# Performance work log

Hardware: AMD Instinct MI355X
Metric: run time of the kernel (lower is better)

The kernel has to match this reference:

```python
import jax, jax.numpy as jnp
import numpy as np

EMBED_DIM = 1024
NUM_HEADS = 16
HEAD_DIM = EMBED_DIM // NUM_HEADS
SCALING = HEAD_DIM ** -0.5
ATTN_CONST = 3.032639477052158
BSZ, SEQ = 4, 1024


def setup_inputs() -> dict:
    key = jax.random.key(0)
    ks = jax.random.split(key, 12)
    s = EMBED_DIM ** -0.5
    return {
        "hidden_states": jax.random.normal(ks[0], (BSZ, SEQ, EMBED_DIM), jnp.float32),
        "attn_input_ids": jax.random.uniform(ks[1], (BSZ * NUM_HEADS, SEQ, SEQ), jnp.float32),
        "Wq": jax.random.normal(ks[2], (EMBED_DIM, EMBED_DIM), jnp.float32) * s,
        "bq": jax.random.normal(ks[3], (EMBED_DIM,), jnp.float32) * 0.02,
        "Wk": jax.random.normal(ks[4], (EMBED_DIM, EMBED_DIM), jnp.float32) * s,
        "bk": jax.random.normal(ks[5], (EMBED_DIM,), jnp.float32) * 0.02,
        "Wv": jax.random.normal(ks[6], (EMBED_DIM, EMBED_DIM), jnp.float32) * s,
        "bv": jax.random.normal(ks[7], (EMBED_DIM,), jnp.float32) * 0.02,
        "Wo": jax.random.normal(ks[8], (EMBED_DIM, EMBED_DIM), jnp.float32) * s,
        "bo": jax.random.normal(ks[9], (EMBED_DIM,), jnp.float32) * 0.02,
    }


def _heads(x, bsz, seq):
    # (b, s, e) -> (b, h, s, d)
    return x.reshape(bsz, seq, NUM_HEADS, HEAD_DIM).transpose(0, 2, 1, 3)


def reference(hidden_states, attn_input_ids, Wq, bq, Wk, bk, Wv, bv, Wo, bo):
    bsz, tgt_len, embed_dim = hidden_states.shape
    # torch nn.Linear: y = x @ W.T + b
    q = (hidden_states @ Wq.T + bq) * SCALING
    k = hidden_states @ Wk.T + bk
    v = hidden_states @ Wv.T + bv
    q = _heads(q, bsz, tgt_len)   # (b,h,t,d)
    k = _heads(k, bsz, tgt_len)
    v = _heads(v, bsz, tgt_len)
    # scores: (b,h,t,s)
    scores = jnp.einsum('bhtd,bhsd->bhts', q, k)
    # additive bias: ATTN_FUNCTION(attn_input_ids) = ATTN_CONST * attn_input_ids
    bias = (ATTN_CONST * attn_input_ids).reshape(bsz, NUM_HEADS, tgt_len, tgt_len)
    attn = jax.nn.softmax(scores + bias, axis=-1)
    # dropout p=0.0 / eval mode -> identity
    out = jnp.einsum('bhts,bhsd->bhtd', attn, v)
    out = out.transpose(0, 2, 1, 3).reshape(bsz, tgt_len, embed_dim)
    return out @ Wo.T + bo
```

## Files before the change

kernel.cpp:

```cpp
#include <hip/hip_runtime.h>
#include <stdint.h>

#define BSZ 4
#define SEQ 1024
#define EMB 1024
#define NH 16
#define HD 64

static constexpr float kScaling   = 0.125f;
static constexpr float kAttnConst = 3.032639477052158f;

using u16 = unsigned short;
typedef __attribute__((ext_vector_type(8))) short  frag8;
typedef __attribute__((ext_vector_type(4))) float  floatx4;
typedef __attribute__((ext_vector_type(4))) u16    u16x4;

__device__ inline float bf2f(u16 v) {
  uint32_t u = ((uint32_t)v) << 16;
  return __builtin_bit_cast(float, u);
}
__device__ inline u16 f2bf(float x) {
  uint32_t u = __builtin_bit_cast(uint32_t, x);
  u += 0x7fffu + ((u >> 16) & 1u);
  return (u16)(u >> 16);
}

__global__ __launch_bounds__(256)
void cvt_kernel(const float* __restrict__ H,
                const float* __restrict__ Wq, const float* __restrict__ Wk,
                const float* __restrict__ Wv, const float* __restrict__ Wo,
                u16* __restrict__ Xb,
                u16* __restrict__ Wqb, u16* __restrict__ Wkb,
                u16* __restrict__ Wvb, u16* __restrict__ Wob)
{
  const size_t base = ((size_t)blockIdx.x * 256 + threadIdx.x) * 4;
  const size_t HN = (size_t)BSZ * SEQ * EMB;
  const size_t WN = (size_t)EMB * EMB;
  const float* src;
  u16* dst;
  size_t off;
  if (base < HN) {
    src = H; dst = Xb; off = base;
  } else {
    const size_t r = base - HN;
    const int w = (int)(r >> 20);
    off = r & (WN - 1);
    src = (w == 0) ? Wq : (w == 1) ? Wk : (w == 2) ? Wv : Wo;
    dst = (w == 0) ? Wqb : (w == 1) ? Wkb : (w == 2) ? Wvb : Wob;
  }
  const float4 v = *reinterpret_cast<const float4*>(src + off);
  u16x4 o;
  o[0] = f2bf(v.x); o[1] = f2bf(v.y); o[2] = f2bf(v.z); o[3] = f2bf(v.w);
  *reinterpret_cast<u16x4*>(dst + off) = o;
}

__device__ inline void gemm_mainloop(const u16* __restrict__ X,
                                     const u16* __restrict__ W,
                                     int m0, int n0,
                                     u16* As, u16* Bs,
                                     floatx4 acc[4][4])
{
  const int tid  = threadIdx.x;
  const int wave = tid >> 6;
  const int lane = tid & 63;
  const int l15  = lane & 15;
  const int quad = lane >> 4;
  const int wr   = (wave >> 1) * 64;
  const int wc   = (wave & 1) * 64;
  const int srow = wave * 32 + (lane >> 3);
  const int scol = (lane & 7) * 8;

  for (int i = 0; i < 4; ++i)
    for (int j = 0; j < 4; ++j)
      acc[i][j] = (floatx4){0.f, 0.f, 0.f, 0.f};

  for (int k0 = 0; k0 < EMB; k0 += 64) {
    for (int i = 0; i < 4; ++i) {
      const u16* ga = X + (size_t)(m0 + srow + i * 8) * EMB + k0 + scol;
      const u16* gb = W + (size_t)(n0 + srow + i * 8) * EMB + k0 + scol;
      u16* la = As + (wave * 4 + i) * 512;
      u16* lb = Bs + (wave * 4 + i) * 512;
      __builtin_amdgcn_global_load_lds(
          (__attribute__((address_space(1))) void*)ga,
          (__attribute__((address_space(3))) void*)la, 16, 0, 0);
      __builtin_amdgcn_global_load_lds(
          (__attribute__((address_space(1))) void*)gb,
          (__attribute__((address_space(3))) void*)lb, 16, 0, 0);
    }
    __syncthreads();
    for (int kc = 0; kc < 2; ++kc) {
      frag8 af[4], bfr[4];
      for (int i = 0; i < 4; ++i)
        af[i] = *reinterpret_cast<const frag8*>(
            As + (wr + i * 16 + l15) * 64 + kc * 32 + quad * 8);
      for (int j = 0; j < 4; ++j)
        bfr[j] = *reinterpret_cast<const frag8*>(
            Bs + (wc + j * 16 + l15) * 64 + kc * 32 + quad * 8);
      for (int i = 0; i < 4; ++i)
        for (int j = 0; j < 4; ++j)
          acc[i][j] = __builtin_amdgcn_mfma_f32_16x16x32_bf16(
              af[i], bfr[j], acc[i][j], 0, 0, 0);
    }
    __syncthreads();
  }
}

__global__ __launch_bounds__(256, 3)
void qkv_kernel(const u16* __restrict__ X,
                const u16* __restrict__ Wqb, const float* __restrict__ bq,
                const u16* __restrict__ Wkb, const float* __restrict__ bk,
                const u16* __restrict__ Wvb, const float* __restrict__ bv,
                u16* __restrict__ Qs, u16* __restrict__ Ks, u16* __restrict__ Vt)
{
  __shared__ __align__(16) u16 As[128 * 64];
  __shared__ __align__(16) u16 Bs[128 * 64];
  const int z  = blockIdx.z;
  const u16*   W  = (z == 0) ? Wqb : (z == 1) ? Wkb : Wvb;
  const float* bb = (z == 0) ? bq  : (z == 1) ? bk  : bv;
  const int m0 = blockIdx.y * 128;
  const int n0 = blockIdx.x * 128;

  floatx4 acc[4][4];
  gemm_mainloop(X, W, m0, n0, As, Bs, acc);

  const int lane = threadIdx.x & 63, l15 = lane & 15, quad = lane >> 4;
  const int wave = threadIdx.x >> 6;
  const int wr = (wave >> 1) * 64, wc = (wave & 1) * 64;

  for (int j = 0; j < 4; ++j) {
    const int   n  = n0 + wc + j * 16 + l15;
    const float bn = bb[n];
    for (int i = 0; i < 4; ++i) {
      const int mbase = m0 + wr + i * 16 + quad * 4;
      if (z == 2) {
        const int b = mbase >> 10, t = mbase & 1023;
        const int h = n >> 6,      d = n & 63;
        u16x4 pk;
        for (int r = 0; r < 4; ++r) pk[r] = f2bf(acc[i][j][r] + bn);
        *reinterpret_cast<u16x4*>(
            Vt + ((size_t)((b * NH + h) * HD + d)) * SEQ + t) = pk;
      } else {
        u16* dst = (z == 0) ? Qs : Ks;
        const float sc = (z == 0) ? kScaling : 1.0f;
        for (int r = 0; r < 4; ++r)
          dst[(size_t)(mbase + r) * EMB + n] = f2bf((acc[i][j][r] + bn) * sc);
      }
    }
  }
}

__global__ __launch_bounds__(256, 4)
void attn_kernel(const u16* __restrict__ Qs, const u16* __restrict__ Ks,
                 const u16* __restrict__ Vt, const float* __restrict__ bias,
                 u16* __restrict__ ctx)
{
  __shared__ __align__(16) u16 Kt[64 * 64];
  __shared__ __align__(16) u16 Vs[64 * 64];
  __shared__ __align__(16) u16 Pbuf[64 * 72];
  const int bh = blockIdx.x;
  const int b  = bh >> 4;
  const int h  = bh & 15;
  const int t0 = blockIdx.y * 64;
  const int wave = threadIdx.x >> 6;
  const int lane = threadIdx.x & 63;
  const int l15 = lane & 15, quad = lane >> 4;
  const int wrow = t0 + wave * 16;
  const int srow = wave * 16 + (lane >> 3);
  const int scol = (lane & 7) * 8;

  frag8 qf[2];
  for (int kc = 0; kc < 2; ++kc)
    qf[kc] = *reinterpret_cast<const frag8*>(
        Qs + (size_t)(b * SEQ + wrow + l15) * EMB + h * HD + kc * 32 + quad * 8);

  floatx4 O[4];
  for (int df = 0; df < 4; ++df) O[df] = (floatx4){0.f, 0.f, 0.f, 0.f};
  float rs[4] = {0.f, 0.f, 0.f, 0.f};

  const float* bline = bias + ((size_t)bh * SEQ + wrow + quad * 4) * SEQ + l15;

  for (int s0 = 0; s0 < SEQ; s0 += 64) {
    for (int i = 0; i < 2; ++i) {
      const u16* gk = Ks + (size_t)(b * SEQ + s0 + srow + i * 8) * EMB + h * HD + scol;
      const u16* gv = Vt + ((size_t)bh * HD + srow + i * 8) * SEQ + s0 + scol;
      __builtin_amdgcn_global_load_lds(
          (__attribute__((address_space(1))) void*)gk,
          (__attribute__((address_space(3))) void*)(Kt + (wave * 2 + i) * 512),
          16, 0, 0);
      __builtin_amdgcn_global_load_lds(
          (__attribute__((address_space(1))) void*)gv,
          (__attribute__((address_space(3))) void*)(Vs + (wave * 2 + i) * 512),
          16, 0, 0);
    }
    float bv[4][4];
    for (int nf = 0; nf < 4; ++nf)
      for (int r = 0; r < 4; ++r)
        bv[nf][r] = __builtin_nontemporal_load(bline + (size_t)r * SEQ + s0 + nf * 16);
    __syncthreads();

    floatx4 S[4];
    __builtin_amdgcn_s_setprio(1);
    for (int nf = 0; nf < 4; ++nf) {
      frag8 k0f = *reinterpret_cast<const frag8*>(
          Kt + (nf * 16 + l15) * 64 + quad * 8);
      frag8 k1f = *reinterpret_cast<const frag8*>(
          Kt + (nf * 16 + l15) * 64 + 32 + quad * 8);
      floatx4 a0 = __builtin_amdgcn_mfma_f32_16x16x32_bf16(
          qf[0], k0f, (floatx4){0.f, 0.f, 0.f, 0.f}, 0, 0, 0);
      S[nf] = __builtin_amdgcn_mfma_f32_16x16x32_bf16(qf[1], k1f, a0, 0, 0, 0);
    }
    __builtin_amdgcn_s_setprio(0);

    for (int nf = 0; nf < 4; ++nf)
      for (int r = 0; r < 4; ++r) {
        const float p = __expf(fmaf(kAttnConst, bv[nf][r], S[nf][r]));
        rs[r] += p;
        Pbuf[(wave * 16 + quad * 4 + r) * 72 + ((nf * 16 + l15) ^ (quad << 4))] =
            f2bf(p);
      }
    asm volatile("s_waitcnt lgkmcnt(0)" ::: "memory");

    frag8 pa[2];
    for (int sc = 0; sc < 2; ++sc)
      pa[sc] = *reinterpret_cast<const frag8*>(
          Pbuf + (wave * 16 + l15) * 72 +
          ((sc * 32 + quad * 8) ^ ((l15 >> 2) << 4)));
    __builtin_amdgcn_s_setprio(1);
    for (int df = 0; df < 4; ++df) {
      frag8 v0f = *reinterpret_cast<const frag8*>(
          Vs + (df * 16 + l15) * 64 + quad * 8);
      frag8 v1f = *reinterpret_cast<const frag8*>(
          Vs + (df * 16 + l15) * 64 + 32 + quad * 8);
      O[df] = __builtin_amdgcn_mfma_f32_16x16x32_bf16(pa[0], v0f, O[df], 0, 0, 0);
      O[df] = __builtin_amdgcn_mfma_f32_16x16x32_bf16(pa[1], v1f, O[df], 0, 0, 0);
    }
    __builtin_amdgcn_s_setprio(0);
    __syncthreads();
  }

  for (int d = 1; d < 16; d <<= 1)
    for (int r = 0; r < 4; ++r)
      rs[r] += __shfl_xor(rs[r], d);

  for (int df = 0; df < 4; ++df)
    for (int r = 0; r < 4; ++r) {
      const int t = wrow + quad * 4 + r;
      ctx[((size_t)(b * SEQ + t)) * EMB + h * HD + df * 16 + l15] =
          f2bf(O[df][r] / rs[r]);
    }
}

__global__ __launch_bounds__(256, 4)
void proj_kernel(const u16* __restrict__ X, const u16* __restrict__ Wob,
                 const float* __restrict__ bo, float* __restrict__ out)
{
  __shared__ __align__(16) u16 As[64 * 64];
  __shared__ __align__(16) u16 Bs[128 * 64];
  const int m0 = blockIdx.y * 64;
  const int n0 = blockIdx.x * 128;

  const int tid  = threadIdx.x;
  const int wave = tid >> 6;
  const int lane = tid & 63;
  const int l15  = lane & 15;
  const int quad = lane >> 4;
  const int wr   = (wave >> 1) * 32;
  const int wc   = (wave & 1) * 64;
  const int srowA = wave * 16 + (lane >> 3);
  const int srowB = wave * 32 + (lane >> 3);
  const int scol  = (lane & 7) * 8;

  floatx4 acc[2][4];
  for (int i = 0; i < 2; ++i)
    for (int j = 0; j < 4; ++j)
      acc[i][j] = (floatx4){0.f, 0.f, 0.f, 0.f};

  for (int k0 = 0; k0 < EMB; k0 += 64) {
    for (int i = 0; i < 2; ++i) {
      const u16* ga = X + (size_t)(m0 + srowA + i * 8) * EMB + k0 + scol;
      __builtin_amdgcn_global_load_lds(
          (__attribute__((address_space(1))) void*)ga,
          (__attribute__((address_space(3))) void*)(As + (wave * 2 + i) * 512),
          16, 0, 0);
    }
    for (int i = 0; i < 4; ++i) {
      const u16* gb = Wob + (size_t)(n0 + srowB + i * 8) * EMB + k0 + scol;
      __builtin_amdgcn_global_load_lds(
          (__attribute__((address_space(1))) void*)gb,
          (__attribute__((address_space(3))) void*)(Bs + (wave * 4 + i) * 512),
          16, 0, 0);
    }
    __syncthreads();
    for (int kc = 0; kc < 2; ++kc) {
      frag8 af[2], bfr[4];
      for (int i = 0; i < 2; ++i)
        af[i] = *reinterpret_cast<const frag8*>(
            As + (wr + i * 16 + l15) * 64 + kc * 32 + quad * 8);
      for (int j = 0; j < 4; ++j)
        bfr[j] = *reinterpret_cast<const frag8*>(
            Bs + (wc + j * 16 + l15) * 64 + kc * 32 + quad * 8);
      for (int i = 0; i < 2; ++i)
        for (int j = 0; j < 4; ++j)
          acc[i][j] = __builtin_amdgcn_mfma_f32_16x16x32_bf16(
              af[i], bfr[j], acc[i][j], 0, 0, 0);
    }
    __syncthreads();
  }

  for (int j = 0; j < 4; ++j) {
    const int   n  = n0 + wc + j * 16 + l15;
    const float bn = bo[n];
    for (int i = 0; i < 2; ++i) {
      const int mbase = m0 + wr + i * 16 + quad * 4;
      for (int r = 0; r < 4; ++r)
        out[(size_t)(mbase + r) * EMB + n] = acc[i][j][r] + bn;
    }
  }
}

extern "C" void kernel_launch(void* const* d_in, const int* in_sizes, int n_in,
                              void* d_out, int out_size, void* d_ws, size_t ws_size,
                              hipStream_t stream)
{
  const float* hidden = (const float*)d_in[0];
  const float* attn_b = (const float*)d_in[1];
  const float* Wq = (const float*)d_in[2];
  const float* bq = (const float*)d_in[3];
  const float* Wk = (const float*)d_in[4];
  const float* bk = (const float*)d_in[5];
  const float* Wv = (const float*)d_in[6];
  const float* bv = (const float*)d_in[7];
  const float* Wo = (const float*)d_in[8];
  const float* bo = (const float*)d_in[9];
  float* out = (float*)d_out;

  const size_t MAT = (size_t)BSZ * SEQ * EMB;
  const size_t WN  = (size_t)EMB * EMB;
  u16* Qs  = (u16*)d_ws;
  u16* Ks  = Qs + MAT;
  u16* Vt  = Ks + MAT;
  u16* ctx = Vt + MAT;
  u16* Xb  = ctx + MAT;
  u16* Wqb = Xb + MAT;
  u16* Wkb = Wqb + WN;
  u16* Wvb = Wkb + WN;
  u16* Wob = Wvb + WN;

  cvt_kernel<<<8192, 256, 0, stream>>>(hidden, Wq, Wk, Wv, Wo,
                                       Xb, Wqb, Wkb, Wvb, Wob);
  qkv_kernel<<<dim3(8, 32, 3), 256, 0, stream>>>(Xb, Wqb, bq, Wkb, bk, Wvb, bv,
                                                 Qs, Ks, Vt);
  attn_kernel<<<dim3(64, 16), 256, 0, stream>>>(Qs, Ks, Vt, attn_b, ctx);
  proj_kernel<<<dim3(8, 64), 256, 0, stream>>>(ctx, Wob, bo, out);
}
```

Baseline: 467.0 us.

## Double attention query tile to 128 rows and stage bias through LDS

The attention kernel now runs 8 waves (512 threads) per block covering 128 query rows. Each K/V tile loaded into LDS is shared by twice as many query rows, and the per-wave K/V load is halved. The additive bias tile is now copied into LDS with async global_load_lds in a swizzled layout instead of per-lane nontemporal register loads, and the Pbuf padding is replaced by XOR swizzling alone. The larger block and the extra 32KB of shared memory reduce the number of resident blocks and the grid size, which risks lower occupancy and weaker latency hiding.

```diff
diff --git a/kernel.cpp b/kernel.cpp
--- a/kernel.cpp
+++ b/kernel.cpp
@@ -149,23 +149,24 @@
   }
 }
 
-__global__ __launch_bounds__(256, 4)
+__global__ __launch_bounds__(512, 4)
 void attn_kernel(const u16* __restrict__ Qs, const u16* __restrict__ Ks,
                  const u16* __restrict__ Vt, const float* __restrict__ bias,
                  u16* __restrict__ ctx)
 {
-  __shared__ __align__(16) u16 Kt[64 * 64];
-  __shared__ __align__(16) u16 Vs[64 * 64];
-  __shared__ __align__(16) u16 Pbuf[64 * 72];
+  __shared__ __align__(16) u16   Kt[64 * 64];
+  __shared__ __align__(16) u16   Vs[64 * 64];
+  __shared__ __align__(16) u16   Pbuf[128 * 64];
+  __shared__ __align__(16) float Bf[128 * 64];
   const int bh = blockIdx.x;
   const int b  = bh >> 4;
   const int h  = bh & 15;
-  const int t0 = blockIdx.y * 64;
+  const int t0 = blockIdx.y * 128;
   const int wave = threadIdx.x >> 6;
   const int lane = threadIdx.x & 63;
   const int l15 = lane & 15, quad = lane >> 4;
   const int wrow = t0 + wave * 16;
-  const int srow = wave * 16 + (lane >> 3);
+  const int srow = wave * 8 + (lane >> 3);
   const int scol = (lane & 7) * 8;
 
   frag8 qf[2];
@@ -177,25 +178,28 @@
   for (int df = 0; df < 4; ++df) O[df] = (floatx4){0.f, 0.f, 0.f, 0.f};
   float rs[4] = {0.f, 0.f, 0.f, 0.f};
 
-  const float* bline = bias + ((size_t)bh * SEQ + wrow + quad * 4) * SEQ + l15;
+  const float* bias_bh = bias + (size_t)bh * SEQ * SEQ;
 
   for (int s0 = 0; s0 < SEQ; s0 += 64) {
-    for (int i = 0; i < 2; ++i) {
-      const u16* gk = Ks + (size_t)(b * SEQ + s0 + srow + i * 8) * EMB + h * HD + scol;
-      const u16* gv = Vt + ((size_t)bh * HD + srow + i * 8) * SEQ + s0 + scol;
+    {
+      const u16* gk = Ks + (size_t)(b * SEQ + s0 + srow) * EMB + h * HD + scol;
+      const u16* gv = Vt + ((size_t)bh * HD + srow) * SEQ + s0 + scol;
       __builtin_amdgcn_global_load_lds(
           (__attribute__((address_space(1))) void*)gk,
-          (__attribute__((address_space(3))) void*)(Kt + (wave * 2 + i) * 512),
+          (__attribute__((address_space(3))) void*)(Kt + wave * 512), 16, 0, 0);
+      __builtin_amdgcn_global_load_lds(
+          (__attribute__((address_space(1))) void*)gv,
+          (__attribute__((address_space(3))) void*)(Vs + wave * 512), 16, 0, 0);
+    }
+    for (int p = 0; p < 4; ++p) {
+      const int row = (wave * 4 + p) * 4 + (lane >> 4);
+      const int col = ((lane & 15) * 4) ^ (p << 4);
+      const float* gsrc = bias_bh + (size_t)(t0 + row) * SEQ + s0 + col;
+      __builtin_amdgcn_global_load_lds(
+          (__attribute__((address_space(1))) void*)gsrc,
+          (__attribute__((address_space(3))) void*)(Bf + (wave * 4 + p) * 256),
           16, 0, 0);
-      __builtin_amdgcn_global_load_lds(
-          (__attribute__((address_space(1))) void*)gv,
-          (__attribute__((address_space(3))) void*)(Vs + (wave * 2 + i) * 512),
-          16, 0, 0);
-    }
-    float bv[4][4];
-    for (int nf = 0; nf < 4; ++nf)
-      for (int r = 0; r < 4; ++r)
-        bv[nf][r] = __builtin_nontemporal_load(bline + (size_t)r * SEQ + s0 + nf * 16);
+    }
     __syncthreads();
 
     floatx4 S[4];
@@ -213,9 +217,11 @@
 
     for (int nf = 0; nf < 4; ++nf)
       for (int r = 0; r < 4; ++r) {
-        const float p = __expf(fmaf(kAttnConst, bv[nf][r], S[nf][r]));
+        const float bvv = Bf[(wave * 16 + quad * 4 + r) * 64 +
+                             ((nf * 16 + l15) ^ (quad << 4))];
+        const float p = __expf(fmaf(kAttnConst, bvv, S[nf][r]));
         rs[r] += p;
-        Pbuf[(wave * 16 + quad * 4 + r) * 72 + ((nf * 16 + l15) ^ (quad << 4))] =
+        Pbuf[(wave * 16 + quad * 4 + r) * 64 + ((nf * 16 + l15) ^ (quad << 4))] =
             f2bf(p);
       }
     asm volatile("s_waitcnt lgkmcnt(0)" ::: "memory");
@@ -223,7 +229,7 @@
     frag8 pa[2];
     for (int sc = 0; sc < 2; ++sc)
       pa[sc] = *reinterpret_cast<const frag8*>(
-          Pbuf + (wave * 16 + l15) * 72 +
+          Pbuf + (wave * 16 + l15) * 64 +
           ((sc * 32 + quad * 8) ^ ((l15 >> 2) << 4)));
     __builtin_amdgcn_s_setprio(1);
     for (int df = 0; df < 4; ++df) {
@@ -350,6 +356,6 @@
                                        Xb, Wqb, Wkb, Wvb, Wob);
   qkv_kernel<<<dim3(8, 32, 3), 256, 0, stream>>>(Xb, Wqb, bq, Wkb, bk, Wvb, bv,
                                                  Qs, Ks, Vt);
-  attn_kernel<<<dim3(64, 16), 256, 0, stream>>>(Qs, Ks, Vt, attn_b, ctx);
+  attn_kernel<<<dim3(64, 8), 512, 0, stream>>>(Qs, Ks, Vt, attn_b, ctx);
   proj_kernel<<<dim3(8, 64), 256, 0, stream>>>(ctx, Wob, bo, out);
 }
```

Result: slower. 492.4 us (+5.4%).

## Double-buffer K/V tiles and prefetch bias one iteration ahead in attention

Applied to the files above, without the earlier changes.

The attention loop now keeps two LDS buffers for K and V. It issues the global-to-LDS loads for the next 64-key tile, plus the next bias values into registers, before computing the current tile, so memory latency overlaps with the MFMA and exp work. The Pbuf row pitch also drops from 72 to 64 to offset the extra LDS from the second K/V buffers. This raises LDS use per block and adds register pressure for the prefetched bias, which may lower occupancy. There is also a risk that the async loads are not properly waited on before the next iteration reads them.

```diff
diff --git a/kernel.cpp b/kernel.cpp
--- a/kernel.cpp
+++ b/kernel.cpp
@@ -154,9 +154,9 @@
                  const u16* __restrict__ Vt, const float* __restrict__ bias,
                  u16* __restrict__ ctx)
 {
-  __shared__ __align__(16) u16 Kt[64 * 64];
-  __shared__ __align__(16) u16 Vs[64 * 64];
-  __shared__ __align__(16) u16 Pbuf[64 * 72];
+  __shared__ __align__(16) u16 Kt[2][64 * 64];
+  __shared__ __align__(16) u16 Vs[2][64 * 64];
+  __shared__ __align__(16) u16 Pbuf[64 * 64];
   const int bh = blockIdx.x;
   const int b  = bh >> 4;
   const int h  = bh & 15;
@@ -178,33 +178,58 @@
   float rs[4] = {0.f, 0.f, 0.f, 0.f};
 
   const float* bline = bias + ((size_t)bh * SEQ + wrow + quad * 4) * SEQ + l15;
-
-  for (int s0 = 0; s0 < SEQ; s0 += 64) {
-    for (int i = 0; i < 2; ++i) {
-      const u16* gk = Ks + (size_t)(b * SEQ + s0 + srow + i * 8) * EMB + h * HD + scol;
-      const u16* gv = Vt + ((size_t)bh * HD + srow + i * 8) * SEQ + s0 + scol;
-      __builtin_amdgcn_global_load_lds(
-          (__attribute__((address_space(1))) void*)gk,
-          (__attribute__((address_space(3))) void*)(Kt + (wave * 2 + i) * 512),
-          16, 0, 0);
-      __builtin_amdgcn_global_load_lds(
-          (__attribute__((address_space(1))) void*)gv,
-          (__attribute__((address_space(3))) void*)(Vs + (wave * 2 + i) * 512),
-          16, 0, 0);
-    }
-    float bv[4][4];
-    for (int nf = 0; nf < 4; ++nf)
-      for (int r = 0; r < 4; ++r)
-        bv[nf][r] = __builtin_nontemporal_load(bline + (size_t)r * SEQ + s0 + nf * 16);
-    __syncthreads();
+  const u16* gk_base = Ks + (size_t)(b * SEQ + srow) * EMB + h * HD + scol;
+  const u16* gv_base = Vt + ((size_t)bh * HD + srow) * SEQ + scol;
+
+  for (int i = 0; i < 2; ++i) {
+    __builtin_amdgcn_global_load_lds(
+        (__attribute__((address_space(1))) void*)(gk_base + (size_t)i * 8 * EMB),
+        (__attribute__((address_space(3))) void*)(Kt[0] + (wave * 2 + i) * 512),
+        16, 0, 0);
+    __builtin_amdgcn_global_load_lds(
+        (__attribute__((address_space(1))) void*)(gv_base + i * 8 * SEQ),
+        (__attribute__((address_space(3))) void*)(Vs[0] + (wave * 2 + i) * 512),
+        16, 0, 0);
+  }
+  float bc[4][4], bn[4][4];
+  for (int nf = 0; nf < 4; ++nf)
+    for (int r = 0; r < 4; ++r)
+      bc[nf][r] = __builtin_nontemporal_load(bline + (size_t)r * SEQ + nf * 16);
+  __syncthreads();
+
+  for (int t = 0; t < 16; ++t) {
+    const int c  = t & 1;
+    const int s0 = t * 64;
+
+    if (t < 15) {
+      const int sn = s0 + 64;
+      for (int i = 0; i < 2; ++i) {
+        __builtin_amdgcn_global_load_lds(
+            (__attribute__((address_space(1))) void*)
+                (gk_base + (size_t)(sn + i * 8) * EMB),
+            (__attribute__((address_space(3))) void*)
+                (Kt[c ^ 1] + (wave * 2 + i) * 512),
+            16, 0, 0);
+        __builtin_amdgcn_global_load_lds(
+            (__attribute__((address_space(1))) void*)
+                (gv_base + i * 8 * SEQ + sn),
+            (__attribute__((address_space(3))) void*)
+                (Vs[c ^ 1] + (wave * 2 + i) * 512),
+            16, 0, 0);
+      }
+      for (int nf = 0; nf < 4; ++nf)
+        for (int r = 0; r < 4; ++r)
+          bn[nf][r] = __builtin_nontemporal_load(
+              bline + (size_t)r * SEQ + sn + nf * 16);
+    }
 
     floatx4 S[4];
     __builtin_amdgcn_s_setprio(1);
     for (int nf = 0; nf < 4; ++nf) {
       frag8 k0f = *reinterpret_cast<const frag8*>(
-          Kt + (nf * 16 + l15) * 64 + quad * 8);
+          Kt[c] + (nf * 16 + l15) * 64 + quad * 8);
       frag8 k1f = *reinterpret_cast<const frag8*>(
-          Kt + (nf * 16 + l15) * 64 + 32 + quad * 8);
+          Kt[c] + (nf * 16 + l15) * 64 + 32 + quad * 8);
       floatx4 a0 = __builtin_amdgcn_mfma_f32_16x16x32_bf16(
           qf[0], k0f, (floatx4){0.f, 0.f, 0.f, 0.f}, 0, 0, 0);
       S[nf] = __builtin_amdgcn_mfma_f32_16x16x32_bf16(qf[1], k1f, a0, 0, 0, 0);
@@ -213,24 +238,27 @@
 
     for (int nf = 0; nf < 4; ++nf)
       for (int r = 0; r < 4; ++r) {
-        const float p = __expf(fmaf(kAttnConst, bv[nf][r], S[nf][r]));
+        const float p = __expf(fmaf(kAttnConst, bc[nf][r], S[nf][r]));
         rs[r] += p;
-        Pbuf[(wave * 16 + quad * 4 + r) * 72 + ((nf * 16 + l15) ^ (quad << 4))] =
+        Pbuf[(wave * 16 + quad * 4 + r) * 64 + ((nf * 16 + l15) ^ (quad << 4))] =
             f2bf(p);
       }
+    if (t < 15)
+      for (int nf = 0; nf < 4; ++nf)
+        for (int r = 0; r < 4; ++r) bc[nf][r] = bn[nf][r];
     asm volatile("s_waitcnt lgkmcnt(0)" ::: "memory");
 
     frag8 pa[2];
     for (int sc = 0; sc < 2; ++sc)
       pa[sc] = *reinterpret_cast<const frag8*>(
-          Pbuf + (wave * 16 + l15) * 72 +
+          Pbuf + (wave * 16 + l15) * 64 +
           ((sc * 32 + quad * 8) ^ ((l15 >> 2) << 4)));
     __builtin_amdgcn_s_setprio(1);
     for (int df = 0; df < 4; ++df) {
       frag8 v0f = *reinterpret_cast<const frag8*>(
-          Vs + (df * 16 + l15) * 64 + quad * 8);
+          Vs[c] + (df * 16 + l15) * 64 + quad * 8);
       frag8 v1f = *reinterpret_cast<const frag8*>(
-          Vs + (df * 16 + l15) * 64 + 32 + quad * 8);
+          Vs[c] + (df * 16 + l15) * 64 + 32 + quad * 8);
       O[df] = __builtin_amdgcn_mfma_f32_16x16x32_bf16(pa[0], v0f, O[df], 0, 0, 0);
       O[df] = __builtin_amdgcn_mfma_f32_16x16x32_bf16(pa[1], v1f, O[df], 0, 0, 0);
     }
```

Result: no change. 468.0 us (+0.2%).
